# Performance work log

Measured on AMD Instinct MI355X. Metric: run time of the kernel, lower is better.

The kernel has to match this reference:

```python
import jax, jax.numpy as jnp
import numpy as np

D_MODEL = 256; D_FF = 512; D_STATE = 16; D_CONV = 4; EXPAND = 2
D_INNER = EXPAND * D_MODEL          # 512
DT_RANK = (D_MODEL + 15) // 16      # 16
BSZ = 16; NVARS = 32; PATCH_NUM = 64


def setup_inputs() -> dict:
    key = jax.random.key(0)
    ks = jax.random.split(key, 16)
    def nrm(k, shape, scale=0.02):
        return jax.random.normal(k, shape, jnp.float32) * scale
    inp = {}
    inp["x"] = jax.random.normal(ks[0], (BSZ, NVARS, D_MODEL, PATCH_NUM), jnp.float32)
    # Mamba block params
    inp["in_proj_w"] = nrm(ks[1], (2 * D_INNER, D_MODEL))
    inp["in_proj_b"] = jnp.zeros((2 * D_INNER,), jnp.float32)
    inp["conv_w"] = nrm(ks[2], (D_INNER, D_CONV), 0.1)   # depthwise causal conv
    inp["conv_b"] = jnp.zeros((D_INNER,), jnp.float32)
    inp["x_proj_w"] = nrm(ks[3], (DT_RANK + 2 * D_STATE, D_INNER))
    inp["dt_proj_w"] = nrm(ks[4], (D_INNER, DT_RANK))
    inp["dt_proj_b"] = nrm(ks[5], (D_INNER,), 0.1)
    inp["A_log"] = jnp.log(jnp.broadcast_to(
        jnp.arange(1, D_STATE + 1, dtype=jnp.float32), (D_INNER, D_STATE)))
    inp["Dp"] = jnp.ones((D_INNER,), jnp.float32)
    inp["out_proj_w"] = nrm(ks[6], (D_MODEL, D_INNER))
    # Mamba_ffn norms + pointwise FFN
    inp["norm1_g"] = jnp.ones((D_MODEL,), jnp.float32)
    inp["norm1_b"] = jnp.zeros((D_MODEL,), jnp.float32)
    inp["ffn1_w"] = nrm(ks[7], (D_FF, D_MODEL))
    inp["ffn1_b"] = jnp.zeros((D_FF,), jnp.float32)
    inp["ffn2_w"] = nrm(ks[8], (D_MODEL, D_FF))
    inp["ffn2_b"] = jnp.zeros((D_MODEL,), jnp.float32)
    inp["norm2_g"] = jnp.ones((D_MODEL,), jnp.float32)
    inp["norm2_b"] = jnp.zeros((D_MODEL,), jnp.float32)
    # outer VarPatch LayerNorm
    inp["ln_g"] = jnp.ones((D_MODEL,), jnp.float32)
    inp["ln_b"] = jnp.zeros((D_MODEL,), jnp.float32)
    return inp


def layer_norm(x, g, b, eps=1e-5):
    mu = x.mean(-1, keepdims=True)
    var = ((x - mu) ** 2).mean(-1, keepdims=True)
    return (x - mu) * jax.lax.rsqrt(var + eps) * g + b


def mamba(x, in_proj_w, in_proj_b, conv_w, conv_b, x_proj_w,
          dt_proj_w, dt_proj_b, A_log, Dp, out_proj_w):
    # x: (b, L, d_model)
    b, L, _ = x.shape
    xz = x @ in_proj_w.T + in_proj_b            # (b, L, 2*d_inner)
    xi, z = jnp.split(xz, 2, axis=-1)           # each (b, L, d_inner)
    # causal depthwise conv along L
    xc = xi.transpose(0, 2, 1)                  # (b, d_inner, L)
    xc = jax.lax.conv_general_dilated(
        xc, conv_w[:, None, :], (1,), [(D_CONV - 1, 0)],
        dimension_numbers=("NCH", "OIH", "NCH"),
        feature_group_count=D_INNER) + conv_b[None, :, None]
    xi = jax.nn.silu(xc.transpose(0, 2, 1))     # (b, L, d_inner)
    x_dbl = xi @ x_proj_w.T                     # (b, L, dt_rank + 2*n)
    dt = x_dbl[..., :DT_RANK]
    B = x_dbl[..., DT_RANK:DT_RANK + D_STATE]
    C = x_dbl[..., DT_RANK + D_STATE:]
    delta = jax.nn.softplus(dt @ dt_proj_w.T + dt_proj_b)   # (b, L, d_inner)
    A = -jnp.exp(A_log)                         # (d_inner, n)

    def step(h, inp):
        d_t, B_t, C_t, u_t = inp                # (b,d),(b,n),(b,n),(b,d)
        dA = jnp.exp(d_t[..., None] * A)        # (b, d, n)
        h = dA * h + (d_t * u_t)[..., None] * B_t[:, None, :]
        y = jnp.einsum("bdn,bn->bd", h, C_t)
        return h, y

    h0 = jnp.zeros((b, D_INNER, D_STATE), xi.dtype)
    xs = (delta.transpose(1, 0, 2), B.transpose(1, 0, 2),
          C.transpose(1, 0, 2), xi.transpose(1, 0, 2))
    _, ys = jax.lax.scan(step, h0, xs)          # ys: (L, b, d_inner)
    y = ys.transpose(1, 0, 2) + xi * Dp
    y = y * jax.nn.silu(z)
    return y @ out_proj_w.T                     # (b, L, d_model)


def reference(x, in_proj_w, in_proj_b, conv_w, conv_b, x_proj_w,
              dt_proj_w, dt_proj_b, A_log, Dp, out_proj_w,
              norm1_g, norm1_b, ffn1_w, ffn1_b, ffn2_w, ffn2_b,
              norm2_g, norm2_b, ln_g, ln_b):
    b, nv, dm, pn = x.shape
    x_residual = x
    h = x.reshape(b, pn * nv, dm)               # same flat view as torch reshape
    # Mamba_ffn: mamba + residual, norm, pointwise FFN + residual, norm
    h = h + mamba(h, in_proj_w, in_proj_b, conv_w, conv_b, x_proj_w,
                  dt_proj_w, dt_proj_b, A_log, Dp, out_proj_w)
    h = layer_norm(h, norm1_g, norm1_b)
    y = jax.nn.relu(h @ ffn1_w.T + ffn1_b)      # 1x1 conv == linear
    y = y @ ffn2_w.T + ffn2_b
    h = layer_norm(h + y, norm2_g, norm2_b)
    # back to patches
    h = h.reshape(b, nv, pn, dm)
    h = layer_norm(h, ln_g, ln_b).transpose(0, 1, 3, 2)   # (b, nv, dm, pn)
    return h + x_residual
```

## Files before the change

kernel.cpp:

```cpp
#include <hip/hip_runtime.h>
#include <hip/hip_bf16.h>
#include <math.h>

#define SEQ    2048
#define NBTOT  16
#define NCH    64
#define CHL    32

#define L2E 1.4426950408889634f

typedef __attribute__((ext_vector_type(8))) __bf16 bf16x8;
typedef __attribute__((ext_vector_type(4))) float f32x4;
typedef __attribute__((ext_vector_type(2))) float f32x2;

#define GLOAD16(gp, lp)                                                   \
  __builtin_amdgcn_global_load_lds(                                       \
      (const __attribute__((address_space(1))) unsigned int*)(gp),        \
      (__attribute__((address_space(3))) unsigned int*)(lp), 16, 0, 0)

__device__ __forceinline__ float exp2_(float x) {
  return __builtin_amdgcn_exp2f(x);
}
__device__ __forceinline__ float silu_(float x) {
  return x * __builtin_amdgcn_rcpf(1.f + exp2_(-x * L2E));
}
__device__ __forceinline__ float softplus_(float x) {
  return fmaxf(x, 0.f) + __logf(1.f + exp2_(-fabsf(x) * L2E));
}
__device__ __forceinline__ float wsum_(float v) {
#pragma unroll
  for (int off = 32; off > 0; off >>= 1) v += __shfl_xor(v, off, 64);
  return v;
}
__device__ __forceinline__ int xcdswz_(int bid, int nwg) {
  return (bid & 7) * (nwg >> 3) + (bid >> 3);
}
__device__ __forceinline__ void powpairs_(float e1, f32x2 p[8]) {
  float e2 = e1 * e1;
  f32x2 p0; p0.x = e1; p0.y = e2;
  f32x2 s2; s2.x = e2; s2.y = e2;
  f32x2 s4 = s2 * s2;
  f32x2 s8 = s4 * s4;
  p[0] = p0;      p[1] = p0 * s2; p[2] = p0 * s4; p[3] = p[1] * s4;
  p[4] = p0 * s8; p[5] = p[1] * s8; p[6] = p[2] * s8; p[7] = p[3] * s8;
}

template <bool BIAS, bool RELU, bool RES, bool RESB, bool F32OUT, bool BF16OUT,
          int NTLOG>
__global__ __launch_bounds__(256) void gemm_bf16(
    const __hip_bfloat16* __restrict__ A, const __hip_bfloat16* __restrict__ W,
    const float* __restrict__ bias, const float* __restrict__ res,
    const __hip_bfloat16* __restrict__ resb, float* __restrict__ C,
    __hip_bfloat16* __restrict__ Cb, int N, int K) {
  __shared__ __align__(16) char ShRaw[36864];
  short* Als = reinterpret_cast<short*>(ShRaw);
  short* Bls = Als + 8192;
  const int tid = threadIdx.x;
  const int lane = tid & 63;
  const int wid = tid >> 6;
  const int swz = xcdswz_(blockIdx.x, gridDim.x);
  const int m0 = (swz >> NTLOG) * 128;
  const int n0 = (swz & ((1 << NTLOG) - 1)) * 128;
  const int wm = (wid >> 1) * 64;
  const int wn = (wid & 1) * 64;
  const int lr = lane & 15;
  const int lk = lane >> 4;

  f32x4 acc[4][4];
#pragma unroll
  for (int m = 0; m < 4; ++m)
#pragma unroll
    for (int n = 0; n < 4; ++n) acc[m][n] = (f32x4){0.f, 0.f, 0.f, 0.f};

  const int srow = wid * 32 + (lane >> 3);
  const int scol = (lane & 7) * 8;
  const __hip_bfloat16* Ag = A + (size_t)(m0 + srow) * K + scol;
  const __hip_bfloat16* Wg = W + (size_t)(n0 + srow) * K + scol;
  short* Alb = Als + wid * 2048;
  short* Blb = Bls + wid * 2048;

  for (int kt = 0; kt < K; kt += 64) {
#pragma unroll
    for (int i = 0; i < 4; ++i) {
      GLOAD16(Ag + (size_t)(i * 8) * K + kt, Alb + i * 512);
      GLOAD16(Wg + (size_t)(i * 8) * K + kt, Blb + i * 512);
    }
    __syncthreads();
    const bf16x8* Af = reinterpret_cast<const bf16x8*>(Als);
    const bf16x8* Bf = reinterpret_cast<const bf16x8*>(Bls);
#pragma unroll
    for (int ks = 0; ks < 2; ++ks) {
      bf16x8 av[4], bv[4];
#pragma unroll
      for (int m = 0; m < 4; ++m)
        av[m] = Af[(wm + m * 16 + lr) * 8 + ks * 4 + lk];
#pragma unroll
      for (int n = 0; n < 4; ++n)
        bv[n] = Bf[(wn + n * 16 + lr) * 8 + ks * 4 + lk];
#pragma unroll
      for (int m = 0; m < 4; ++m)
#pragma unroll
        for (int n = 0; n < 4; ++n)
          acc[m][n] = __builtin_amdgcn_mfma_f32_16x16x32_bf16(
              av[m], bv[n], acc[m][n], 0, 0, 0);
    }
    __syncthreads();
  }

  if (BF16OUT) {
    __hip_bfloat16* epi =
        reinterpret_cast<__hip_bfloat16*>(ShRaw) + wid * 4608;
#pragma unroll
    for (int n = 0; n < 4; ++n) {
      int col = n0 + wn + n * 16 + lr;
      float bval = BIAS ? bias[col] : 0.f;
#pragma unroll
      for (int m = 0; m < 4; ++m) {
        int lrow = m * 16 + lk * 4;
#pragma unroll
        for (int r = 0; r < 4; ++r) {
          float v = acc[m][n][r];
          if (BIAS) v += bval;
          if (RES) v += res[(size_t)(m0 + wm + lrow + r) * N + col];
          if (RESB)
            v += __bfloat162float(resb[(size_t)(m0 + wm + lrow + r) * N + col]);
          if (RELU) v = fmaxf(v, 0.f);
          epi[(lrow + r) * 72 + n * 16 + lr] = __float2bfloat16(v);
        }
      }
    }
    const int lr8 = (lane & 7) * 8;
    const int lrw = lane >> 3;
    const size_t obase = (size_t)(m0 + wm) * N + n0 + wn + lr8;
#pragma unroll
    for (int j = 0; j < 8; ++j) {
      int row = j * 8 + lrw;
      int4 vv = *reinterpret_cast<const int4*>(epi + row * 72 + lr8);
      *reinterpret_cast<int4*>(&Cb[obase + (size_t)row * N]) = vv;
    }
  }
  if (F32OUT) {
#pragma unroll
    for (int n = 0; n < 4; ++n) {
      int col = n0 + wn + n * 16 + lr;
      if (col >= N) continue;
      float bval = BIAS ? bias[col] : 0.f;
#pragma unroll
      for (int m = 0; m < 4; ++m) {
        int row0 = m0 + wm + m * 16 + lk * 4;
#pragma unroll
        for (int r = 0; r < 4; ++r) {
          size_t off = (size_t)(row0 + r) * N + col;
          float v = acc[m][n][r];
          if (BIAS) v += bval;
          if (RES) v += res[off];
          if (RESB) v += __bfloat162float(resb[off]);
          if (RELU) v = fmaxf(v, 0.f);
          C[off] = v;
        }
      }
    }
  }
}

__global__ __launch_bounds__(256) void cast_bf16_k(
    const float* __restrict__ src, __hip_bfloat16* __restrict__ dst, int n4) {
  int i = xcdswz_(blockIdx.x, gridDim.x) * 256 + threadIdx.x;
  if (i >= n4) return;
  float4 v = reinterpret_cast<const float4*>(src)[i];
  union { __hip_bfloat16 h[4]; short4 s4; } u;
  u.h[0] = __float2bfloat16(v.x); u.h[1] = __float2bfloat16(v.y);
  u.h[2] = __float2bfloat16(v.z); u.h[3] = __float2bfloat16(v.w);
  reinterpret_cast<short4*>(dst)[i] = u.s4;
}

__global__ __launch_bounds__(256) void pad_wx_k(
    const float* __restrict__ src, __hip_bfloat16* __restrict__ dst) {
  int i = blockIdx.x * 256 + threadIdx.x;
  int row = i >> 7;
  union { __hip_bfloat16 h[4]; short4 s4; } u;
  if (row < 48) {
    float4 v = reinterpret_cast<const float4*>(src)[i];
    u.h[0] = __float2bfloat16(v.x); u.h[1] = __float2bfloat16(v.y);
    u.h[2] = __float2bfloat16(v.z); u.h[3] = __float2bfloat16(v.w);
  } else {
    u.h[0] = u.h[1] = u.h[2] = u.h[3] = __float2bfloat16(0.f);
  }
  reinterpret_cast<short4*>(dst)[i] = u.s4;
}

__global__ __launch_bounds__(256) void conv_silu_k(
    const __hip_bfloat16* __restrict__ xz, const float* __restrict__ cw,
    const float* __restrict__ cb, __hip_bfloat16* __restrict__ xi) {
  int idx = xcdswz_(blockIdx.x, gridDim.x) * 256 + threadIdx.x;
  int t = idx & 63;
  int rp = idx >> 6;
  int r = rp << 1;
  int l = r & (SEQ - 1);
  int c8 = t << 3;
  const __hip_bfloat16* p = xz + (size_t)r * 1024 + c8;
  union U8 { int4 v; __hip_bfloat16 h[8]; } x0, x1, x2, x3, x4, oa, ob;
  const int4 z4 = make_int4(0, 0, 0, 0);
  x4.v = *reinterpret_cast<const int4*>(p + 1024);
  x3.v = *reinterpret_cast<const int4*>(p);
  x2.v = (l >= 1) ? *reinterpret_cast<const int4*>(p - 1024) : z4;
  x1.v = (l >= 2) ? *reinterpret_cast<const int4*>(p - 2048) : z4;
  x0.v = (l >= 3) ? *reinterpret_cast<const int4*>(p - 3072) : z4;
  const float4* cw4 = reinterpret_cast<const float4*>(cw);
#pragma unroll
  for (int j = 0; j < 8; ++j) {
    float4 w = cw4[c8 + j];
    float b = cb[c8 + j];
    float f0 = __bfloat162float(x0.h[j]);
    float f1 = __bfloat162float(x1.h[j]);
    float f2 = __bfloat162float(x2.h[j]);
    float f3 = __bfloat162float(x3.h[j]);
    float f4 = __bfloat162float(x4.h[j]);
    float a0 = fmaf(w.w, f3, fmaf(w.z, f2, fmaf(w.y, f1, fmaf(w.x, f0, b))));
    float a1 = fmaf(w.w, f4, fmaf(w.z, f3, fmaf(w.y, f2, fmaf(w.x, f1, b))));
    oa.h[j] = __float2bfloat16(silu_(a0));
    ob.h[j] = __float2bfloat16(silu_(a1));
  }
  *reinterpret_cast<int4*>(&xi[(size_t)r * 512 + c8]) = oa.v;
  *reinterpret_cast<int4*>(&xi[(size_t)(r + 1) * 512 + c8]) = ob.v;
}

__global__ __launch_bounds__(256) void scan_p1(
    const __hip_bfloat16* __restrict__ u, const float* __restrict__ xdbl,
    const float* __restrict__ A_log, const float* __restrict__ wdt,
    const float* __restrict__ bdt, float* __restrict__ dlsum,
    __hip_bfloat16* __restrict__ hp, __hip_bfloat16* __restrict__ deltab) {
  const int w = xcdswz_(blockIdx.x, gridDim.x);
  const int b = w >> 7;
  const int c = (w >> 1) & 63;
  const int d = ((w & 1) << 8) + threadIdx.x;
  const int l0 = c * CHL;
  float A2[16];
  f32x2 w2[8];
  {
    const float4* aq = reinterpret_cast<const float4*>(&A_log[d * 16]);
    const f32x2* wq = reinterpret_cast<const f32x2*>(&wdt[d * 16]);
#pragma unroll
    for (int q = 0; q < 4; ++q) {
      float4 v = aq[q];
      A2[q * 4 + 0] = -exp2_(v.x * L2E) * L2E;
      A2[q * 4 + 1] = -exp2_(v.y * L2E) * L2E;
      A2[q * 4 + 2] = -exp2_(v.z * L2E) * L2E;
      A2[q * 4 + 3] = -exp2_(v.w * L2E) * L2E;
    }
#pragma unroll
    for (int k = 0; k < 8; ++k) w2[k] = wq[k];
  }
  bool chainok = true;
#pragma unroll
  for (int n = 1; n < 16; ++n)
    chainok = chainok &&
              (fabsf(A2[n] - (float)(n + 1) * A2[0]) <=
               1e-4f * (float)(n + 1) * fabsf(A2[0]));
  const float bdtd = bdt[d];
  const float nL = A2[0];
  f32x2 h2[8];
#pragma unroll
  for (int k = 0; k < 8; ++k) h2[k] = (f32x2){0.f, 0.f};
  float dls = 0.f;
  size_t base = (size_t)(b * SEQ + l0) * 512 + d;
  const float* rowp = xdbl + (size_t)(b * SEQ + l0) * 48;
  if (chainok) {
#pragma unroll 4
    for (int i = 0; i < CHL; ++i) {
      const f32x2* r2 = reinterpret_cast<const f32x2*>(rowp + i * 48);
      f32x2 acc2; acc2.x = bdtd; acc2.y = 0.f;
#pragma unroll
      for (int k = 0; k < 8; ++k)
        acc2 = __builtin_elementwise_fma(r2[k], w2[k], acc2);
      float dl = softplus_(acc2.x + acc2.y);
      deltab[base + (size_t)i * 512] = __float2bfloat16(dl);
      dls += dl;
      float du = dl * __bfloat162float(u[base + (size_t)i * 512]);
      f32x2 p[8];
      powpairs_(exp2_(dl * nL), p);
      f32x2 du2; du2.x = du; du2.y = du;
#pragma unroll
      for (int k = 0; k < 8; ++k)
        h2[k] = __builtin_elementwise_fma(p[k], h2[k], du2 * r2[8 + k]);
    }
  } else {
#pragma unroll 2
    for (int i = 0; i < CHL; ++i) {
      const f32x2* r2 = reinterpret_cast<const f32x2*>(rowp + i * 48);
      f32x2 acc2; acc2.x = bdtd; acc2.y = 0.f;
#pragma unroll
      for (int k = 0; k < 8; ++k)
        acc2 = __builtin_elementwise_fma(r2[k], w2[k], acc2);
      float dl = softplus_(acc2.x + acc2.y);
      deltab[base + (size_t)i * 512] = __float2bfloat16(dl);
      dls += dl;
      float du = dl * __bfloat162float(u[base + (size_t)i * 512]);
      f32x2 du2; du2.x = du; du2.y = du;
#pragma unroll
      for (int k = 0; k < 8; ++k) {
        f32x2 a; a.x = exp2_(dl * A2[2 * k]); a.y = exp2_(dl * A2[2 * k + 1]);
        h2[k] = __builtin_elementwise_fma(a, h2[k], du2 * r2[8 + k]);
      }
    }
  }
  size_t sc = (size_t)(b * NCH + c) * 512 + d;
  dlsum[sc] = dls;
  union { __hip_bfloat16 h[4]; short4 s4; } o0, o1, o2, o3;
#pragma unroll
  for (int j = 0; j < 2; ++j) {
    o0.h[2*j] = __float2bfloat16(h2[j].x);   o0.h[2*j+1] = __float2bfloat16(h2[j].y);
    o1.h[2*j] = __float2bfloat16(h2[2+j].x); o1.h[2*j+1] = __float2bfloat16(h2[2+j].y);
    o2.h[2*j] = __float2bfloat16(h2[4+j].x); o2.h[2*j+1] = __float2bfloat16(h2[4+j].y);
    o3.h[2*j] = __float2bfloat16(h2[6+j].x); o3.h[2*j+1] = __float2bfloat16(h2[6+j].y);
  }
  short4* hq = reinterpret_cast<short4*>(hp + sc * 16);
  hq[0] = o0.s4; hq[1] = o1.s4; hq[2] = o2.s4; hq[3] = o3.s4;
}

__global__ __launch_bounds__(256) void scan_p2(
    __hip_bfloat16* hp, const float* __restrict__ dlsum,
    const float* __restrict__ A_log) {
  int g = xcdswz_(blockIdx.x, gridDim.x) * 256 + threadIdx.x;
  int b = g >> 13;
  int dn = g & 8191;
  int d = dn >> 4;
  float A2n = -exp2_(A_log[dn] * L2E) * L2E;
  float H = 0.f;
  for (int c = 0; c < NCH; ++c) {
    float ds = dlsum[(size_t)(b * NCH + c) * 512 + d];
    size_t idx = (size_t)(b * NCH + c) * 8192 + dn;
    float p = __bfloat162float(hp[idx]);
    float a = exp2_(A2n * ds);
    hp[idx] = __float2bfloat16(H);
    H = fmaf(a, H, p);
  }
}

__global__ __launch_bounds__(256) void scan_p3(
    const __hip_bfloat16* u,
    const float* __restrict__ A_log,
    const __hip_bfloat16* __restrict__ deltab, const float* __restrict__ xdbl,
    const __hip_bfloat16* __restrict__ Hc, const float* __restrict__ Dp,
    const __hip_bfloat16* __restrict__ xz, __hip_bfloat16* y) {
  const int w = xcdswz_(blockIdx.x, gridDim.x);
  const int b = w >> 7;
  const int c = (w >> 1) & 63;
  const int d = ((w & 1) << 8) + threadIdx.x;
  const int l0 = c * CHL;
  float A2[16];
  {
    const float4* aq = reinterpret_cast<const float4*>(&A_log[d * 16]);
#pragma unroll
    for (int q = 0; q < 4; ++q) {
      float4 v = aq[q];
      A2[q * 4 + 0] = -exp2_(v.x * L2E) * L2E;
      A2[q * 4 + 1] = -exp2_(v.y * L2E) * L2E;
      A2[q * 4 + 2] = -exp2_(v.z * L2E) * L2E;
      A2[q * 4 + 3] = -exp2_(v.w * L2E) * L2E;
    }
  }
  bool chainok = true;
#pragma unroll
  for (int n = 1; n < 16; ++n)
    chainok = chainok &&
              (fabsf(A2[n] - (float)(n + 1) * A2[0]) <=
               1e-4f * (float)(n + 1) * fabsf(A2[0]));
  const float nL = A2[0];
  f32x2 h2[8];
  {
    const short4* hq =
        reinterpret_cast<const short4*>(Hc + ((size_t)(b * NCH + c) * 512 + d) * 16);
#pragma unroll
    for (int q = 0; q < 4; ++q) {
      union { short4 s4; __hip_bfloat16 h[4]; } iv;
      iv.s4 = hq[q];
      h2[2*q].x = __bfloat162float(iv.h[0]);
      h2[2*q].y = __bfloat162float(iv.h[1]);
      h2[2*q+1].x = __bfloat162float(iv.h[2]);
      h2[2*q+1].y = __bfloat162float(iv.h[3]);
    }
  }
  const float Dpd = Dp[d];
  size_t base = (size_t)(b * SEQ + l0) * 512 + d;
  const float* rowp = xdbl + (size_t)(b * SEQ + l0) * 48;
  const __hip_bfloat16* zp = xz + (size_t)(b * SEQ + l0) * 1024 + 512 + d;
  if (chainok) {
#pragma unroll 4
    for (int i = 0; i < CHL; ++i) {
      const f32x2* r2 = reinterpret_cast<const f32x2*>(rowp + i * 48);
      float dl = __bfloat162float(deltab[base + (size_t)i * 512]);
      float ul = __bfloat162float(u[base + (size_t)i * 512]);
      float du = dl * ul;
      f32x2 p[8];
      powpairs_(exp2_(dl * nL), p);
      f32x2 du2; du2.x = du; du2.y = du;
      f32x2 yv2; yv2.x = 0.f; yv2.y = 0.f;
#pragma unroll
      for (int k = 0; k < 8; ++k) {
        h2[k] = __builtin_elementwise_fma(p[k], h2[k], du2 * r2[8 + k]);
        yv2 = __builtin_elementwise_fma(h2[k], r2[16 + k], yv2);
      }
      float yv = yv2.x + yv2.y;
      float zv = __bfloat162float(zp[(size_t)i * 1024]);
      y[base + (size_t)i * 512] =
          __float2bfloat16((yv + ul * Dpd) * silu_(zv));
    }
  } else {
#pragma unroll 2
    for (int i = 0; i < CHL; ++i) {
      const f32x2* r2 = reinterpret_cast<const f32x2*>(rowp + i * 48);
      float dl = __bfloat162float(deltab[base + (size_t)i * 512]);
      float ul = __bfloat162float(u[base + (size_t)i * 512]);
      float du = dl * ul;
      f32x2 du2; du2.x = du; du2.y = du;
      f32x2 yv2; yv2.x = 0.f; yv2.y = 0.f;
#pragma unroll
      for (int k = 0; k < 8; ++k) {
        f32x2 a; a.x = exp2_(dl * A2[2 * k]); a.y = exp2_(dl * A2[2 * k + 1]);
        h2[k] = __builtin_elementwise_fma(a, h2[k], du2 * r2[8 + k]);
        yv2 = __builtin_elementwise_fma(h2[k], r2[16 + k], yv2);
      }
      float yv = yv2.x + yv2.y;
      float zv = __bfloat162float(zp[(size_t)i * 1024]);
      y[base + (size_t)i * 512] =
          __float2bfloat16((yv + ul * Dpd) * silu_(zv));
    }
  }
}

__global__ __launch_bounds__(256) void ln_k(
    const __hip_bfloat16* __restrict__ in, const float* __restrict__ g,
    const float* __restrict__ bb, __hip_bfloat16* __restrict__ outb) {
  int row = (xcdswz_(blockIdx.x, gridDim.x) * 256 + threadIdx.x) >> 6;
  int lane = threadIdx.x & 63;
  union { short4 s4; __hip_bfloat16 h[4]; } iv;
  iv.s4 = reinterpret_cast<const short4*>(in)[row * 64 + lane];
  float v0 = __bfloat162float(iv.h[0]), v1 = __bfloat162float(iv.h[1]);
  float v2 = __bfloat162float(iv.h[2]), v3 = __bfloat162float(iv.h[3]);
  float mu = wsum_(v0 + v1 + v2 + v3) * (1.f / 256.f);
  float a0 = v0 - mu, a1 = v1 - mu, a2 = v2 - mu, a3 = v3 - mu;
  float var = wsum_(a0 * a0 + a1 * a1 + a2 * a2 + a3 * a3) * (1.f / 256.f);
  float rs = __builtin_amdgcn_rsqf(var + 1e-5f);
  float4 gg = *reinterpret_cast<const float4*>(&g[lane * 4]);
  float4 bq = *reinterpret_cast<const float4*>(&bb[lane * 4]);
  union { __hip_bfloat16 h[4]; short4 s4; } u;
  u.h[0] = __float2bfloat16(a0 * rs * gg.x + bq.x);
  u.h[1] = __float2bfloat16(a1 * rs * gg.y + bq.y);
  u.h[2] = __float2bfloat16(a2 * rs * gg.z + bq.z);
  u.h[3] = __float2bfloat16(a3 * rs * gg.w + bq.w);
  reinterpret_cast<short4*>(outb)[row * 64 + lane] = u.s4;
}

__global__ __launch_bounds__(256) void final_k(
    const __hip_bfloat16* __restrict__ t2, const float* __restrict__ g2v,
    const float* __restrict__ b2v, const float* __restrict__ g3v,
    const float* __restrict__ b3v, const __hip_bfloat16* __restrict__ xbf,
    float* __restrict__ out) {
  int bx = xcdswz_(blockIdx.x, gridDim.x);
  int half = bx & 1, nv = (bx >> 1) & 31, b = bx >> 6;
  int wave = threadIdx.x >> 6, lane = threadIdx.x & 63;
  __shared__ float sh[32][257];
  float4 gg2 = *reinterpret_cast<const float4*>(&g2v[lane * 4]);
  float4 bb2 = *reinterpret_cast<const float4*>(&b2v[lane * 4]);
  float4 gg3 = *reinterpret_cast<const float4*>(&g3v[lane * 4]);
  float4 bb3 = *reinterpret_cast<const float4*>(&b3v[lane * 4]);
#pragma unroll
  for (int i = 0; i < 8; ++i) {
    int pn = wave * 8 + i;
    int r = ((b * 32 + nv) << 6) + (half << 5) + pn;
    union { short4 s4; __hip_bfloat16 h[4]; } iv;
    iv.s4 = reinterpret_cast<const short4*>(t2)[r * 64 + lane];
    float v0 = __bfloat162float(iv.h[0]), v1 = __bfloat162float(iv.h[1]);
    float v2 = __bfloat162float(iv.h[2]), v3 = __bfloat162float(iv.h[3]);
    float mu = wsum_(v0 + v1 + v2 + v3) * (1.f / 256.f);
    float a0 = v0 - mu, a1 = v1 - mu, a2 = v2 - mu, a3 = v3 - mu;
    float var = wsum_(a0 * a0 + a1 * a1 + a2 * a2 + a3 * a3) * (1.f / 256.f);
    float rs = __builtin_amdgcn_rsqf(var + 1e-5f);
    a0 = a0 * rs * gg2.x + bb2.x; a1 = a1 * rs * gg2.y + bb2.y;
    a2 = a2 * rs * gg2.z + bb2.z; a3 = a3 * rs * gg2.w + bb2.w;
    mu = wsum_(a0 + a1 + a2 + a3) * (1.f / 256.f);
    float c0 = a0 - mu, c1 = a1 - mu, c2 = a2 - mu, c3 = a3 - mu;
    var = wsum_(c0 * c0 + c1 * c1 + c2 * c2 + c3 * c3) * (1.f / 256.f);
    rs = __builtin_amdgcn_rsqf(var + 1e-5f);
    sh[pn][lane * 4 + 0] = c0 * rs * gg3.x + bb3.x;
    sh[pn][lane * 4 + 1] = c1 * rs * gg3.y + bb3.y;
    sh[pn][lane * 4 + 2] = c2 * rs * gg3.z + bb3.z;
    sh[pn][lane * 4 + 3] = c3 * rs * gg3.w + bb3.w;
  }
  __syncthreads();
  int pnl = threadIdx.x & 31;
  int dbase = threadIdx.x >> 5;
  size_t obase = (size_t)((b * 32 + nv) * 256) * 64 + (half << 5) + pnl;
#pragma unroll
  for (int k = 0; k < 32; ++k) {
    int dd = dbase + (k << 3);
    size_t oi = obase + (size_t)dd * 64;
    out[oi] = sh[pnl][dd] + __bfloat162float(xbf[oi]);
  }
}

extern "C" void kernel_launch(void* const* d_in, const int* in_sizes, int n_in,
                              void* d_out, int out_size, void* d_ws,
                              size_t ws_size, hipStream_t stream) {
  const float* x    = (const float*)d_in[0];
  const float* w_in = (const float*)d_in[1];
  const float* b_in = (const float*)d_in[2];
  const float* cw   = (const float*)d_in[3];
  const float* cb   = (const float*)d_in[4];
  const float* wx   = (const float*)d_in[5];
  const float* wdt  = (const float*)d_in[6];
  const float* bdt  = (const float*)d_in[7];
  const float* alog = (const float*)d_in[8];
  const float* Dp   = (const float*)d_in[9];
  const float* wout = (const float*)d_in[10];
  const float* g1   = (const float*)d_in[11];
  const float* b1   = (const float*)d_in[12];
  const float* wf1  = (const float*)d_in[13];
  const float* bf1  = (const float*)d_in[14];
  const float* wf2  = (const float*)d_in[15];
  const float* bf2  = (const float*)d_in[16];
  const float* g2   = (const float*)d_in[17];
  const float* b2   = (const float*)d_in[18];
  const float* g3   = (const float*)d_in[19];
  const float* b3   = (const float*)d_in[20];
  float* out = (float*)d_out;

  const size_t MB1 = 1048576;
  char* g = (char*)d_ws;
  __hip_bfloat16* wbf_in  = (__hip_bfloat16*)(g);
  __hip_bfloat16* wbf_out = (__hip_bfloat16*)(g + 524288);
  __hip_bfloat16* wbf_f1  = (__hip_bfloat16*)(g + 786432);
  __hip_bfloat16* wbf_f2  = (__hip_bfloat16*)(g + 1048576);
  __hip_bfloat16* wbf_xp  = (__hip_bfloat16*)(g + 1310720);
  const size_t SHARED = 1572864;

  const size_t PB = 11 * MB1 + 393216 + 131072;
  int nb = (int)((ws_size - SHARED) / PB);
  if (ws_size <= SHARED || nb < 1) return;
  if (nb > NBTOT) nb = NBTOT;

  dim3 blk(256);
  cast_bf16_k<<<dim3(256), blk, 0, stream>>>(w_in, wbf_in, 65536);
  cast_bf16_k<<<dim3(128), blk, 0, stream>>>(wout, wbf_out, 32768);
  cast_bf16_k<<<dim3(128), blk, 0, stream>>>(wf1, wbf_f1, 32768);
  cast_bf16_k<<<dim3(128), blk, 0, stream>>>(wf2, wbf_f2, 32768);
  pad_wx_k<<<dim3(64), blk, 0, stream>>>(wx, wbf_xp);

  for (int b0 = 0; b0 < NBTOT; b0 += nb) {
    int bn = (NBTOT - b0 < nb) ? (NBTOT - b0) : nb;
    char* base = g + SHARED;
    char* RA = base;
    char* RB = base + (size_t)bn * 4 * MB1;
    char* RC = base + (size_t)bn * 5 * MB1;
    char* RD = base + (size_t)bn * 7 * MB1;
    char* RE = RD + (size_t)bn * 393216;
    char* RF = RE + (size_t)bn * 2 * MB1;
    char* RG = RF + (size_t)bn * 2 * MB1;

    __hip_bfloat16* xz     = (__hip_bfloat16*)RA;
    __hip_bfloat16* t2b    = (__hip_bfloat16*)RA;
    __hip_bfloat16* xbf    = (__hip_bfloat16*)RB;
    __hip_bfloat16* xibf   = (__hip_bfloat16*)RC;
    __hip_bfloat16* ffnybf = (__hip_bfloat16*)RC;
    float*          xdbl   = (float*)RD;
    __hip_bfloat16* hp     = (__hip_bfloat16*)RE;
    __hip_bfloat16* resb   = (__hip_bfloat16*)RE;
    __hip_bfloat16* h1bf   = (__hip_bfloat16*)(RE + (size_t)bn * MB1);
    __hip_bfloat16* deltab = (__hip_bfloat16*)RF;
    float*          dlsum  = (float*)RG;

    const float* xg = x + (size_t)b0 * SEQ * 256;
    float* outg = out + (size_t)b0 * SEQ * 256;
    int M = bn * SEQ;
    int MT = M / 128;

    cast_bf16_k<<<dim3(M * 64 / 256), blk, 0, stream>>>(xg, xbf, M * 64);
    gemm_bf16<true, false, false, false, false, true, 3>
        <<<dim3(8 * MT), blk, 0, stream>>>(xbf, wbf_in, b_in, nullptr, nullptr,
                                           nullptr, xz, 1024, 256);
    conv_silu_k<<<dim3(M / 8), blk, 0, stream>>>(xz, cw, cb, xibf);
    gemm_bf16<false, false, false, false, true, false, 0>
        <<<dim3(MT), blk, 0, stream>>>(xibf, wbf_xp, nullptr, nullptr,
                                       nullptr, xdbl, nullptr, 48, 512);
    scan_p1<<<dim3(bn * 128), blk, 0, stream>>>(xibf, xdbl, alog, wdt, bdt,
                                                dlsum, hp, deltab);
    scan_p2<<<dim3(bn * 32), blk, 0, stream>>>(hp, dlsum, alog);
    scan_p3<<<dim3(bn * 128), blk, 0, stream>>>(xibf, alog, deltab, xdbl,
                                                hp, Dp, xz, xibf);
    gemm_bf16<false, false, false, true, false, true, 1>
        <<<dim3(2 * MT), blk, 0, stream>>>(xibf, wbf_out, nullptr, nullptr,
                                           xbf, nullptr, resb, 256, 512);
    ln_k<<<dim3(M / 4), blk, 0, stream>>>(resb, g1, b1, h1bf);
    gemm_bf16<true, true, false, false, false, true, 2>
        <<<dim3(4 * MT), blk, 0, stream>>>(h1bf, wbf_f1, bf1, nullptr, nullptr,
                                           nullptr, ffnybf, 512, 256);
    gemm_bf16<true, false, false, true, false, true, 1>
        <<<dim3(2 * MT), blk, 0, stream>>>(ffnybf, wbf_f2, bf2, nullptr, h1bf,
                                           nullptr, t2b, 256, 512);
    final_k<<<dim3(bn * 64), blk, 0, stream>>>(t2b, g2, b2, g3, b3, xbf, outg);
  }
}
```

Measured before the change: 260.2 us.

## Compute dt projection and softplus with a bf16 MFMA GEMM instead of inside scan

```diff
diff --git a/kernel.cpp b/kernel.cpp
--- a/kernel.cpp
+++ b/kernel.cpp
@@ -46,12 +46,13 @@
 }
 
 template <bool BIAS, bool RELU, bool RES, bool RESB, bool F32OUT, bool BF16OUT,
-          int NTLOG>
+          bool SOFTPLUS, bool DTOUT, int NTLOG>
 __global__ __launch_bounds__(256) void gemm_bf16(
     const __hip_bfloat16* __restrict__ A, const __hip_bfloat16* __restrict__ W,
     const float* __restrict__ bias, const float* __restrict__ res,
     const __hip_bfloat16* __restrict__ resb, float* __restrict__ C,
-    __hip_bfloat16* __restrict__ Cb, int N, int K) {
+    __hip_bfloat16* __restrict__ Cb, __hip_bfloat16* __restrict__ dtb,
+    int N, int K) {
   __shared__ __align__(16) char ShRaw[36864];
   short* Als = reinterpret_cast<short*>(ShRaw);
   short* Bls = Als + 8192;
@@ -125,6 +126,7 @@
           if (RESB)
             v += __bfloat162float(resb[(size_t)(m0 + wm + lrow + r) * N + col]);
           if (RELU) v = fmaxf(v, 0.f);
+          if (SOFTPLUS) v = softplus_(v);
           epi[(lrow + r) * 72 + n * 16 + lr] = __float2bfloat16(v);
         }
       }
@@ -161,6 +163,23 @@
       }
     }
   }
+  if (DTOUT) {
+    if (wn == 0) {
+#pragma unroll
+      for (int n = 0; n < 4; ++n) {
+        int col = n * 16 + lr;
+#pragma unroll
+        for (int m = 0; m < 4; ++m) {
+          int row0 = m0 + wm + m * 16 + lk * 4;
+#pragma unroll
+          for (int r = 0; r < 4; ++r) {
+            float v = (col < 16) ? acc[m][n][r] : 0.f;
+            dtb[(size_t)(row0 + r) * 64 + col] = __float2bfloat16(v);
+          }
+        }
+      }
+    }
+  }
 }
 
 __global__ __launch_bounds__(256) void cast_bf16_k(
@@ -181,6 +200,22 @@
   union { __hip_bfloat16 h[4]; short4 s4; } u;
   if (row < 48) {
     float4 v = reinterpret_cast<const float4*>(src)[i];
+    u.h[0] = __float2bfloat16(v.x); u.h[1] = __float2bfloat16(v.y);
+    u.h[2] = __float2bfloat16(v.z); u.h[3] = __float2bfloat16(v.w);
+  } else {
+    u.h[0] = u.h[1] = u.h[2] = u.h[3] = __float2bfloat16(0.f);
+  }
+  reinterpret_cast<short4*>(dst)[i] = u.s4;
+}
+
+__global__ __launch_bounds__(256) void pad_wdt_k(
+    const float* __restrict__ src, __hip_bfloat16* __restrict__ dst) {
+  int i = blockIdx.x * 256 + threadIdx.x;
+  int row = i >> 4;
+  int cq = (i & 15) * 4;
+  union { __hip_bfloat16 h[4]; short4 s4; } u;
+  if (cq < 16) {
+    float4 v = *reinterpret_cast<const float4*>(&src[row * 16 + cq]);
     u.h[0] = __float2bfloat16(v.x); u.h[1] = __float2bfloat16(v.y);
     u.h[2] = __float2bfloat16(v.z); u.h[3] = __float2bfloat16(v.w);
   } else {
@@ -227,19 +262,17 @@
 
 __global__ __launch_bounds__(256) void scan_p1(
     const __hip_bfloat16* __restrict__ u, const float* __restrict__ xdbl,
-    const float* __restrict__ A_log, const float* __restrict__ wdt,
-    const float* __restrict__ bdt, float* __restrict__ dlsum,
-    __hip_bfloat16* __restrict__ hp, __hip_bfloat16* __restrict__ deltab) {
+    const float* __restrict__ A_log,
+    const __hip_bfloat16* __restrict__ deltab, float* __restrict__ dlsum,
+    __hip_bfloat16* __restrict__ hp) {
   const int w = xcdswz_(blockIdx.x, gridDim.x);
   const int b = w >> 7;
   const int c = (w >> 1) & 63;
   const int d = ((w & 1) << 8) + threadIdx.x;
   const int l0 = c * CHL;
   float A2[16];
-  f32x2 w2[8];
   {
     const float4* aq = reinterpret_cast<const float4*>(&A_log[d * 16]);
-    const f32x2* wq = reinterpret_cast<const f32x2*>(&wdt[d * 16]);
 #pragma unroll
     for (int q = 0; q < 4; ++q) {
       float4 v = aq[q];
@@ -248,8 +281,6 @@
       A2[q * 4 + 2] = -exp2_(v.z * L2E) * L2E;
       A2[q * 4 + 3] = -exp2_(v.w * L2E) * L2E;
     }
-#pragma unroll
-    for (int k = 0; k < 8; ++k) w2[k] = wq[k];
   }
   bool chainok = true;
 #pragma unroll
@@ -257,7 +288,6 @@
     chainok = chainok &&
               (fabsf(A2[n] - (float)(n + 1) * A2[0]) <=
                1e-4f * (float)(n + 1) * fabsf(A2[0]));
-  const float bdtd = bdt[d];
   const float nL = A2[0];
   f32x2 h2[8];
 #pragma unroll
@@ -269,12 +299,7 @@
 #pragma unroll 4
     for (int i = 0; i < CHL; ++i) {
       const f32x2* r2 = reinterpret_cast<const f32x2*>(rowp + i * 48);
-      f32x2 acc2; acc2.x = bdtd; acc2.y = 0.f;
-#pragma unroll
-      for (int k = 0; k < 8; ++k)
-        acc2 = __builtin_elementwise_fma(r2[k], w2[k], acc2);
-      float dl = softplus_(acc2.x + acc2.y);
-      deltab[base + (size_t)i * 512] = __float2bfloat16(dl);
+      float dl = __bfloat162float(deltab[base + (size_t)i * 512]);
       dls += dl;
       float du = dl * __bfloat162float(u[base + (size_t)i * 512]);
       f32x2 p[8];
@@ -288,12 +313,7 @@
 #pragma unroll 2
     for (int i = 0; i < CHL; ++i) {
       const f32x2* r2 = reinterpret_cast<const f32x2*>(rowp + i * 48);
-      f32x2 acc2; acc2.x = bdtd; acc2.y = 0.f;
-#pragma unroll
-      for (int k = 0; k < 8; ++k)
-        acc2 = __builtin_elementwise_fma(r2[k], w2[k], acc2);
-      float dl = softplus_(acc2.x + acc2.y);
-      deltab[base + (size_t)i * 512] = __float2bfloat16(dl);
+      float dl = __bfloat162float(deltab[base + (size_t)i * 512]);
       dls += dl;
       float du = dl * __bfloat162float(u[base + (size_t)i * 512]);
       f32x2 du2; du2.x = du; du2.y = du;
@@ -533,9 +553,10 @@
   __hip_bfloat16* wbf_f1  = (__hip_bfloat16*)(g + 786432);
   __hip_bfloat16* wbf_f2  = (__hip_bfloat16*)(g + 1048576);
   __hip_bfloat16* wbf_xp  = (__hip_bfloat16*)(g + 1310720);
+  __hip_bfloat16* wdtb    = (__hip_bfloat16*)(g + 1441792);
   const size_t SHARED = 1572864;
 
-  const size_t PB = 11 * MB1 + 393216 + 131072;
+  const size_t PB = 11 * MB1 + 393216 + 131072 + 262144;
   int nb = (int)((ws_size - SHARED) / PB);
   if (ws_size <= SHARED || nb < 1) return;
   if (nb > NBTOT) nb = NBTOT;
@@ -546,6 +567,7 @@
   cast_bf16_k<<<dim3(128), blk, 0, stream>>>(wf1, wbf_f1, 32768);
   cast_bf16_k<<<dim3(128), blk, 0, stream>>>(wf2, wbf_f2, 32768);
   pad_wx_k<<<dim3(64), blk, 0, stream>>>(wx, wbf_xp);
+  pad_wdt_k<<<dim3(32), blk, 0, stream>>>(wdt, wdtb);
 
   for (int b0 = 0; b0 < NBTOT; b0 += nb) {
     int bn = (NBTOT - b0 < nb) ? (NBTOT - b0) : nb;
@@ -557,6 +579,7 @@
     char* RE = RD + (size_t)bn * 393216;
     char* RF = RE + (size_t)bn * 2 * MB1;
     char* RG = RF + (size_t)bn * 2 * MB1;
+    char* RH = RG + (size_t)bn * 131072;
 
     __hip_bfloat16* xz     = (__hip_bfloat16*)RA;
     __hip_bfloat16* t2b    = (__hip_bfloat16*)RA;
@@ -569,6 +592,7 @@
     __hip_bfloat16* h1bf   = (__hip_bfloat16*)(RE + (size_t)bn * MB1);
     __hip_bfloat16* deltab = (__hip_bfloat16*)RF;
     float*          dlsum  = (float*)RG;
+    __hip_bfloat16* dtb    = (__hip_bfloat16*)RH;
 
     const float* xg = x + (size_t)b0 * SEQ * 256;
     float* outg = out + (size_t)b0 * SEQ * 256;
@@ -576,28 +600,32 @@
     int MT = M / 128;
 
     cast_bf16_k<<<dim3(M * 64 / 256), blk, 0, stream>>>(xg, xbf, M * 64);
-    gemm_bf16<true, false, false, false, false, true, 3>
+    gemm_bf16<true, false, false, false, false, true, false, false, 3>
         <<<dim3(8 * MT), blk, 0, stream>>>(xbf, wbf_in, b_in, nullptr, nullptr,
-                                           nullptr, xz, 1024, 256);
+                                           nullptr, xz, nullptr, 1024, 256);
     conv_silu_k<<<dim3(M / 8), blk, 0, stream>>>(xz, cw, cb, xibf);
-    gemm_bf16<false, false, false, false, true, false, 0>
-        <<<dim3(MT), blk, 0, stream>>>(xibf, wbf_xp, nullptr, nullptr,
-                                       nullptr, xdbl, nullptr, 48, 512);
-    scan_p1<<<dim3(bn * 128), blk, 0, stream>>>(xibf, xdbl, alog, wdt, bdt,
-                                                dlsum, hp, deltab);
+    gemm_bf16<false, false, false, false, true, false, false, true, 0>
+        <<<dim3(MT), blk, 0, stream>>>(xibf, wbf_xp, nullptr, nullptr, nullptr,
+                                       xdbl, nullptr, dtb, 48, 512);
+    gemm_bf16<true, false, false, false, false, true, true, false, 2>
+        <<<dim3(4 * MT), blk, 0, stream>>>(dtb, wdtb, bdt, nullptr, nullptr,
+                                           nullptr, deltab, nullptr, 512, 64);
+    scan_p1<<<dim3(bn * 128), blk, 0, stream>>>(xibf, xdbl, alog, deltab,
+                                                dlsum, hp);
     scan_p2<<<dim3(bn * 32), blk, 0, stream>>>(hp, dlsum, alog);
     scan_p3<<<dim3(bn * 128), blk, 0, stream>>>(xibf, alog, deltab, xdbl,
                                                 hp, Dp, xz, xibf);
-    gemm_bf16<false, false, false, true, false, true, 1>
+    gemm_bf16<false, false, false, true, false, true, false, false, 1>
         <<<dim3(2 * MT), blk, 0, stream>>>(xibf, wbf_out, nullptr, nullptr,
-                                           xbf, nullptr, resb, 256, 512);
+                                           xbf, nullptr, resb, nullptr,
+                                           256, 512);
     ln_k<<<dim3(M / 4), blk, 0, stream>>>(resb, g1, b1, h1bf);
-    gemm_bf16<true, true, false, false, false, true, 2>
+    gemm_bf16<true, true, false, false, false, true, false, false, 2>
         <<<dim3(4 * MT), blk, 0, stream>>>(h1bf, wbf_f1, bf1, nullptr, nullptr,
-                                           nullptr, ffnybf, 512, 256);
-    gemm_bf16<true, false, false, true, false, true, 1>
+                                           nullptr, ffnybf, nullptr, 512, 256);
+    gemm_bf16<true, false, false, true, false, true, false, false, 1>
         <<<dim3(2 * MT), blk, 0, stream>>>(ffnybf, wbf_f2, bf2, nullptr, h1bf,
-                                           nullptr, t2b, 256, 512);
+                                           nullptr, t2b, nullptr, 256, 512);
     final_k<<<dim3(bn * 64), blk, 0, stream>>>(t2b, g2, b2, g3, b3, xbf, outg);
   }
 }
```

Measured after the change: 269.0 us. 3.4% more time.
